# Kernel optimization log

Measured on AMD Instinct MI355X. Metric: run time of the kernel, lower is better.

Reference implementation:

```python
import jax, jax.numpy as jnp
import numpy as np

B, S, D, H = 4, 2048, 512, 8
HD = D // H

def setup_inputs() -> dict:
    key = jax.random.key(0)
    ks = jax.random.split(key, 11)
    sc = 0.02
    inp = {
        'query': jax.random.normal(ks[0], (B, S, D), jnp.float32),
        'key':   jax.random.normal(ks[1], (B, S, D), jnp.float32),
        'value': jax.random.normal(ks[2], (B, S, D), jnp.float32),
        # causal boolean mask, broadcastable to (B, H, S, S)
        'mask':  jnp.tril(jnp.ones((S, S), bool))[None, None],
        'wq': jax.random.normal(ks[3], (D, D), jnp.float32) * sc,
        'bq': jnp.zeros((D,), jnp.float32),
        'wk': jax.random.normal(ks[4], (D, D), jnp.float32) * sc,
        'bk': jnp.zeros((D,), jnp.float32),
        'wv': jax.random.normal(ks[5], (D, D), jnp.float32) * sc,
        'bv': jnp.zeros((D,), jnp.float32),
        'wo': jax.random.normal(ks[6], (D, D), jnp.float32) * sc,
        'bo': jnp.zeros((D,), jnp.float32),
    }
    return inp


def reference(query, key, value, mask, wq, bq, wk, bk, wv, bv, wo, bo):
    b, s, d = query.shape

    def proj(x, w, bias):
        # torch nn.Linear: x @ W^T + b, then split heads -> (B, H, L, HD)
        y = x @ w.T + bias
        return y.reshape(b, -1, H, HD).transpose(0, 2, 1, 3)

    q = proj(query, wq, bq)   # (B,H,S,HD)
    k = proj(key,   wk, bk)
    v = proj(value, wv, bv)

    scores = jnp.einsum('bhqd,bhkd->bhqk', q, k) / np.sqrt(HD).astype(jnp.float32)
    scores = jnp.where(mask, scores, -jnp.inf)
    # torch code subtracts rowmax then softmaxes; jax.nn.softmax is the same stable form
    attn = jax.nn.softmax(scores, axis=-1)  # dropout p=0.0 -> identity
    out = jnp.einsum('bhqk,bhkd->bhqd', attn, v)
    out = out.transpose(0, 2, 1, 3).reshape(b, s, d)
    return out @ wo.T + bo
```

## Files before the change

kernel.cpp:

```cpp
#include <hip/hip_runtime.h>

#define NB 4
#define NS 2048
#define ND 512
#define NH 8
#define NHD 64
#define NM (NB*NS)

using bf16 = __bf16;
using bf16x8 = __bf16 __attribute__((ext_vector_type(8)));
using f32x4 = float __attribute__((ext_vector_type(4)));
using i16x4 = short __attribute__((ext_vector_type(4)));

static_assert(sizeof(bf16x8) == 16, "bf16x8 must be 16B");
static_assert(sizeof(i16x4) == 8, "i16x4 must be 8B");

typedef __attribute__((address_space(1))) void glob_t;
typedef __attribute__((address_space(3))) void lds_t;

__device__ __forceinline__ void mfma16(f32x4& c, i16x4 a, i16x4 b) {
    asm("v_mfma_f32_16x16x16_bf16 %0, %1, %2, %0" : "+v"(c) : "v"(a), "v"(b));
}

__device__ __forceinline__ void stage16_f32(const float* __restrict__ src, bf16* dst) {
    float4 f0 = *(const float4*)(src + 0);
    float4 f1 = *(const float4*)(src + 4);
    float4 f2 = *(const float4*)(src + 8);
    float4 f3 = *(const float4*)(src + 12);
    bf16x8 v0, v1;
    v0[0]=(bf16)f0.x; v0[1]=(bf16)f0.y; v0[2]=(bf16)f0.z; v0[3]=(bf16)f0.w;
    v0[4]=(bf16)f1.x; v0[5]=(bf16)f1.y; v0[6]=(bf16)f1.z; v0[7]=(bf16)f1.w;
    v1[0]=(bf16)f2.x; v1[1]=(bf16)f2.y; v1[2]=(bf16)f2.z; v1[3]=(bf16)f2.w;
    v1[4]=(bf16)f3.x; v1[5]=(bf16)f3.y; v1[6]=(bf16)f3.z; v1[7]=(bf16)f3.w;
    *(bf16x8*)dst       = v0;
    *(bf16x8*)(dst + 8) = v1;
}

template<bool A_BF16, bool HEAD_OUT>
__device__ __forceinline__ void gemm_body(bf16* As, bf16* Bs, const void* __restrict__ Ap,
        const float* __restrict__ W, const float* __restrict__ bias, void* __restrict__ outp)
{
    constexpr int LP = 40;
    const int tid  = threadIdx.x;
    const int lane = tid & 63;
    const int wid  = tid >> 6;
    const int wm = wid >> 1, wn = wid & 1;
    const int lr = lane & 15, lg = lane >> 4;
    const int m0 = blockIdx.x * 128, n0 = blockIdx.y * 128;

    const int srow = tid >> 1;
    const int scol = (tid & 1) << 4;

    f32x4 acc[4][4] = {};

    for (int k0 = 0; k0 < ND; k0 += 32) {
        if (A_BF16) {
            const bf16* src = (const bf16*)Ap + (size_t)(m0 + srow) * ND + k0 + scol;
            *(uint4*)&As[srow * LP + scol]     = *(const uint4*)(src);
            *(uint4*)&As[srow * LP + scol + 8] = *(const uint4*)(src + 8);
        } else {
            const float* src = (const float*)Ap + (size_t)(m0 + srow) * ND + k0 + scol;
            stage16_f32(src, &As[srow * LP + scol]);
        }
        {
            const float* src = W + (size_t)(n0 + srow) * ND + k0 + scol;
            stage16_f32(src, &Bs[srow * LP + scol]);
        }
        __syncthreads();

        bf16x8 af[4], bfr[4];
        #pragma unroll
        for (int i = 0; i < 4; i++)
            af[i] = *(const bf16x8*)&As[(wm * 64 + i * 16 + lr) * LP + lg * 8];
        #pragma unroll
        for (int i = 0; i < 4; i++)
            bfr[i] = *(const bf16x8*)&Bs[(wn * 64 + i * 16 + lr) * LP + lg * 8];

        #pragma unroll
        for (int mf = 0; mf < 4; mf++)
            #pragma unroll
            for (int nf = 0; nf < 4; nf++)
                acc[mf][nf] = __builtin_amdgcn_mfma_f32_16x16x32_bf16(
                        af[mf], bfr[nf], acc[mf][nf], 0, 0, 0);
        __syncthreads();
    }

    float bv[4];
    #pragma unroll
    for (int nf = 0; nf < 4; nf++)
        bv[nf] = bias[n0 + wn * 64 + nf * 16 + lr];

    #pragma unroll
    for (int mf = 0; mf < 4; mf++) {
        #pragma unroll
        for (int nf = 0; nf < 4; nf++) {
            const int col = n0 + wn * 64 + nf * 16 + lr;
            #pragma unroll
            for (int r = 0; r < 4; r++) {
                const int row = m0 + wm * 64 + mf * 16 + lg * 4 + r;
                const float v = acc[mf][nf][r] + bv[nf];
                if (HEAD_OUT) {
                    const int b  = row >> 11;
                    const int s  = row & (NS - 1);
                    const int hh = col >> 6;
                    const int hd = col & (NHD - 1);
                    ((bf16*)outp)[(((size_t)b * NH + hh) * NS + s) * NHD + hd] = (bf16)v;
                } else {
                    ((float*)outp)[(size_t)row * ND + col] = v;
                }
            }
        }
    }
}

__global__ __launch_bounds__(256) void gemm_proj3(
        const float* __restrict__ q, const float* __restrict__ k, const float* __restrict__ v,
        const float* __restrict__ wq, const float* __restrict__ wk, const float* __restrict__ wv,
        const float* __restrict__ bq, const float* __restrict__ bk, const float* __restrict__ bv,
        bf16* __restrict__ qb, bf16* __restrict__ kb, bf16* __restrict__ vb)
{
    __shared__ __align__(16) bf16 As[128 * 40];
    __shared__ __align__(16) bf16 Bs[128 * 40];
    const int z = blockIdx.z;
    const float* A = (z == 0) ? q  : (z == 1) ? k  : v;
    const float* W = (z == 0) ? wq : (z == 1) ? wk : wv;
    const float* B = (z == 0) ? bq : (z == 1) ? bk : bv;
    bf16*        o = (z == 0) ? qb : (z == 1) ? kb : vb;
    gemm_body<false, true>(As, Bs, A, W, B, o);
}

__global__ __launch_bounds__(256) void gemm_out(const bf16* __restrict__ A,
        const float* __restrict__ W, const float* __restrict__ b, float* __restrict__ out)
{
    __shared__ __align__(16) bf16 As[128 * 40];
    __shared__ __align__(16) bf16 Bs[128 * 40];
    gemm_body<true, false>(As, Bs, A, W, b, out);
}

#define QSCALE 0.18033688011112042f

__global__ __launch_bounds__(128) void attn_kern(const bf16* __restrict__ Qg,
        const bf16* __restrict__ Kg, const bf16* __restrict__ Vg,
        bf16* __restrict__ Og)
{
    __shared__ __align__(16) bf16 Kt[2][64 * 64];
    __shared__ __align__(16) bf16 Vt[2][64 * 64];

    const int b = blockIdx.z, h = blockIdx.y;
    const int x = blockIdx.x;
    const int qb = (x & 1) ? ((x - 1) >> 1) : (31 - (x >> 1));
    const int tid = threadIdx.x;
    const int lane = tid & 63, w = tid >> 6;
    const int lr = lane & 15, lg = lane >> 4;

    const size_t bh = ((size_t)b * NH + h) * NS;
    const bf16* Kb = Kg + bh * NHD;
    const bf16* Vb = Vg + bh * NHD;

    int ksrc[4];
    #pragma unroll
    for (int j = 0; j < 4; j++) {
        const int c   = (w * 4 + j) * 64 + lane;
        const int row = c >> 3;
        const int cs  = (c & 7) ^ (row & 7);
        ksrc[j] = row * NHD + cs * 8;
    }

    const int c8 = tid >> 4;
    const int r0 = (tid & 15) * 4;

    bf16x8 qf[2][2];
    #pragma unroll
    for (int rf = 0; rf < 2; rf++) {
        const bf16* qp = Qg + (bh + qb * 64 + w * 32 + rf * 16 + lr) * NHD;
        #pragma unroll
        for (int kk = 0; kk < 2; kk++) {
            bf16x8 t = *(const bf16x8*)(qp + kk * 32 + lg * 8);
            #pragma unroll
            for (int j = 0; j < 8; j++)
                qf[rf][kk][j] = (bf16)((float)t[j] * QSCALE);
        }
    }

    f32x4 acc_o[2][4] = {};
    float l_lane[2] = {0.f, 0.f};

    const int qrow0 = qb * 64 + w * 32;
    const int ntiles = qb + 1;

    auto stage = [&](int buf, int kv0) {
        #pragma unroll
        for (int j = 0; j < 4; j++)
            __builtin_amdgcn_global_load_lds(
                (const glob_t*)(Kb + (size_t)kv0 * NHD + ksrc[j]),
                (lds_t*)(&Kt[buf][(w * 4 + j) * 512]), 16, 0, 0);
        bf16x8 vv[4];
        #pragma unroll
        for (int i = 0; i < 4; i++)
            vv[i] = *(const bf16x8*)(Vb + (size_t)(kv0 + r0 + i) * NHD + c8 * 8);
        #pragma unroll
        for (int j = 0; j < 8; j++) {
            const int hd = c8 * 8 + j;
            int byte = hd * 128 + r0 * 2;
            byte ^= (hd & 7) << 4;
            i16x4 pk;
            #pragma unroll
            for (int i = 0; i < 4; i++) {
                bf16 hval = vv[i][j];
                pk[i] = (short)__builtin_bit_cast(unsigned short, hval);
            }
            *(i16x4*)((char*)&Vt[buf][0] + byte) = pk;
        }
    };

    stage(0, 0);
    __syncthreads();

    int cur = 0;
    for (int t = 0; t < ntiles; t++) {
        const int kv0 = t * 64;
        if (t + 1 < ntiles) stage(cur ^ 1, kv0 + 64);

        f32x4 s[4][2];
        #pragma unroll
        for (int nf = 0; nf < 4; nf++) {
            bf16x8 kf[2];
            #pragma unroll
            for (int kk = 0; kk < 2; kk++) {
                const int row = nf * 16 + lr;
                int byte = row * 128 + (kk * 32 + lg * 8) * 2;
                byte ^= (row & 7) << 4;
                kf[kk] = *(const bf16x8*)((const char*)&Kt[cur][0] + byte);
            }
            #pragma unroll
            for (int rf = 0; rf < 2; rf++) {
                f32x4 a = {};
                a = __builtin_amdgcn_mfma_f32_16x16x32_bf16(kf[0], qf[rf][0], a, 0, 0, 0);
                a = __builtin_amdgcn_mfma_f32_16x16x32_bf16(kf[1], qf[rf][1], a, 0, 0, 0);
                s[nf][rf] = a;
            }
        }

        i16x4 pa[2][4];
        if (kv0 + 63 > qrow0) {
            #pragma unroll
            for (int rf = 0; rf < 2; rf++) {
                const int qg = qrow0 + rf * 16 + lr;
                #pragma unroll
                for (int nf = 0; nf < 4; nf++)
                    #pragma unroll
                    for (int rr = 0; rr < 4; rr++) {
                        const int kvg = kv0 + nf * 16 + lg * 4 + rr;
                        float sv = s[nf][rf][rr];
                        sv = (kvg > qg) ? -1e30f : sv;
                        const float p = __builtin_amdgcn_exp2f(sv);
                        l_lane[rf] += p;
                        bf16 ph = (bf16)p;
                        pa[rf][nf][rr] = (short)__builtin_bit_cast(unsigned short, ph);
                    }
            }
        } else {
            #pragma unroll
            for (int rf = 0; rf < 2; rf++)
                #pragma unroll
                for (int nf = 0; nf < 4; nf++)
                    #pragma unroll
                    for (int rr = 0; rr < 4; rr++) {
                        const float p = __builtin_amdgcn_exp2f(s[nf][rf][rr]);
                        l_lane[rf] += p;
                        bf16 ph = (bf16)p;
                        pa[rf][nf][rr] = (short)__builtin_bit_cast(unsigned short, ph);
                    }
        }

        i16x4 vf[4][4];
        #pragma unroll
        for (int hf = 0; hf < 4; hf++)
            #pragma unroll
            for (int nf = 0; nf < 4; nf++) {
                const int hd = hf * 16 + lr;
                int byte = hd * 128 + (nf * 16 + lg * 4) * 2;
                byte ^= (hd & 7) << 4;
                vf[hf][nf] = *(const i16x4*)((const char*)&Vt[cur][0] + byte);
            }

        __builtin_amdgcn_s_setprio(1);
        #pragma unroll
        for (int rf = 0; rf < 2; rf++)
            #pragma unroll
            for (int hf = 0; hf < 4; hf++)
                #pragma unroll
                for (int nf = 0; nf < 4; nf++)
                    mfma16(acc_o[rf][hf], pa[rf][nf], vf[hf][nf]);
        __builtin_amdgcn_s_setprio(0);

        __syncthreads();
        cur ^= 1;
    }

    #pragma unroll
    for (int rf = 0; rf < 2; rf++) {
        float l = l_lane[rf];
        l += __shfl_xor(l, 16);
        l += __shfl_xor(l, 32);
        const float linv = 1.0f / l;
        #pragma unroll
        for (int rr = 0; rr < 4; rr++) {
            const float li = __shfl(linv, lg * 4 + rr, 16);
            const int row = qrow0 + rf * 16 + lg * 4 + rr;
            #pragma unroll
            for (int hf = 0; hf < 4; hf++) {
                const int col = h * NHD + hf * 16 + lr;
                Og[((size_t)b * NS + row) * ND + col] = (bf16)(acc_o[rf][hf][rr] * li);
            }
        }
    }
}

extern "C" void kernel_launch(void* const* d_in, const int* in_sizes, int n_in,
                              void* d_out, int out_size, void* d_ws, size_t ws_size,
                              hipStream_t stream) {
    const float* query = (const float*)d_in[0];
    const float* key   = (const float*)d_in[1];
    const float* value = (const float*)d_in[2];
    const float* wq = (const float*)d_in[4];
    const float* bq = (const float*)d_in[5];
    const float* wk = (const float*)d_in[6];
    const float* bk = (const float*)d_in[7];
    const float* wv = (const float*)d_in[8];
    const float* bv = (const float*)d_in[9];
    const float* wo = (const float*)d_in[10];
    const float* bo = (const float*)d_in[11];
    float* out = (float*)d_out;

    bf16* qb = (bf16*)d_ws;
    bf16* kb = qb + (size_t)NM * ND;
    bf16* vb = kb + (size_t)NM * ND;
    bf16* ob = vb + (size_t)NM * ND;

    gemm_proj3<<<dim3(NM / 128, ND / 128, 3), 256, 0, stream>>>(
            query, key, value, wq, wk, wv, bq, bk, bv, qb, kb, vb);

    attn_kern<<<dim3(NS / 64, NH, NB), 128, 0, stream>>>(qb, kb, vb, ob);

    gemm_out<<<dim3(NM / 128, ND / 128), 256, 0, stream>>>(ob, wo, bo, out);
}
```

Baseline: 127.1 us.

## Double-buffer GEMM shared-memory tiles with register prefetch of next K tile

The projection and output GEMMs now prefetch the next K-slice of A and W into registers while MFMAs run on the current LDS buffer, then convert and write into the alternate LDS buffer. This cuts one of the two barriers per iteration and hides global load latency behind compute. It doubles LDS use per block and adds register pressure from the prefetched float4 values, which could lower occupancy.

```diff
diff --git a/kernel.cpp b/kernel.cpp
--- a/kernel.cpp
+++ b/kernel.cpp
@@ -22,16 +22,12 @@
     asm("v_mfma_f32_16x16x16_bf16 %0, %1, %2, %0" : "+v"(c) : "v"(a), "v"(b));
 }
 
-__device__ __forceinline__ void stage16_f32(const float* __restrict__ src, bf16* dst) {
-    float4 f0 = *(const float4*)(src + 0);
-    float4 f1 = *(const float4*)(src + 4);
-    float4 f2 = *(const float4*)(src + 8);
-    float4 f3 = *(const float4*)(src + 12);
+__device__ __forceinline__ void cvt16(const float4* f, bf16* dst) {
     bf16x8 v0, v1;
-    v0[0]=(bf16)f0.x; v0[1]=(bf16)f0.y; v0[2]=(bf16)f0.z; v0[3]=(bf16)f0.w;
-    v0[4]=(bf16)f1.x; v0[5]=(bf16)f1.y; v0[6]=(bf16)f1.z; v0[7]=(bf16)f1.w;
-    v1[0]=(bf16)f2.x; v1[1]=(bf16)f2.y; v1[2]=(bf16)f2.z; v1[3]=(bf16)f2.w;
-    v1[4]=(bf16)f3.x; v1[5]=(bf16)f3.y; v1[6]=(bf16)f3.z; v1[7]=(bf16)f3.w;
+    v0[0]=(bf16)f[0].x; v0[1]=(bf16)f[0].y; v0[2]=(bf16)f[0].z; v0[3]=(bf16)f[0].w;
+    v0[4]=(bf16)f[1].x; v0[5]=(bf16)f[1].y; v0[6]=(bf16)f[1].z; v0[7]=(bf16)f[1].w;
+    v1[0]=(bf16)f[2].x; v1[1]=(bf16)f[2].y; v1[2]=(bf16)f[2].z; v1[3]=(bf16)f[2].w;
+    v1[4]=(bf16)f[3].x; v1[5]=(bf16)f[3].y; v1[6]=(bf16)f[3].z; v1[7]=(bf16)f[3].w;
     *(bf16x8*)dst       = v0;
     *(bf16x8*)(dst + 8) = v1;
 }
@@ -40,7 +36,8 @@
 __device__ __forceinline__ void gemm_body(bf16* As, bf16* Bs, const void* __restrict__ Ap,
         const float* __restrict__ W, const float* __restrict__ bias, void* __restrict__ outp)
 {
-    constexpr int LP = 40;
+    constexpr int LP  = 40;
+    constexpr int BUF = 128 * LP;
     const int tid  = threadIdx.x;
     const int lane = tid & 63;
     const int wid  = tid >> 6;
@@ -53,28 +50,55 @@
 
     f32x4 acc[4][4] = {};
 
-    for (int k0 = 0; k0 < ND; k0 += 32) {
+    float4 fa[4], fb[4];
+    uint4  ua[2];
+
+    auto load_tile = [&](int k0) {
         if (A_BF16) {
             const bf16* src = (const bf16*)Ap + (size_t)(m0 + srow) * ND + k0 + scol;
-            *(uint4*)&As[srow * LP + scol]     = *(const uint4*)(src);
-            *(uint4*)&As[srow * LP + scol + 8] = *(const uint4*)(src + 8);
+            ua[0] = *(const uint4*)(src);
+            ua[1] = *(const uint4*)(src + 8);
         } else {
             const float* src = (const float*)Ap + (size_t)(m0 + srow) * ND + k0 + scol;
-            stage16_f32(src, &As[srow * LP + scol]);
-        }
-        {
-            const float* src = W + (size_t)(n0 + srow) * ND + k0 + scol;
-            stage16_f32(src, &Bs[srow * LP + scol]);
-        }
-        __syncthreads();
+            fa[0] = *(const float4*)(src + 0);
+            fa[1] = *(const float4*)(src + 4);
+            fa[2] = *(const float4*)(src + 8);
+            fa[3] = *(const float4*)(src + 12);
+        }
+        const float* wsrc = W + (size_t)(n0 + srow) * ND + k0 + scol;
+        fb[0] = *(const float4*)(wsrc + 0);
+        fb[1] = *(const float4*)(wsrc + 4);
+        fb[2] = *(const float4*)(wsrc + 8);
+        fb[3] = *(const float4*)(wsrc + 12);
+    };
+    auto write_tile = [&](int buf) {
+        bf16* da = As + buf * BUF + srow * LP + scol;
+        if (A_BF16) {
+            *(uint4*)da       = ua[0];
+            *(uint4*)(da + 8) = ua[1];
+        } else {
+            cvt16(fa, da);
+        }
+        cvt16(fb, Bs + buf * BUF + srow * LP + scol);
+    };
+
+    load_tile(0);
+    write_tile(0);
+    __syncthreads();
+
+    int cur = 0;
+    #pragma unroll 2
+    for (int t = 0; t < ND / 32; t++) {
+        const int k0 = t * 32;
+        if (t < ND / 32 - 1) load_tile(k0 + 32);
 
         bf16x8 af[4], bfr[4];
         #pragma unroll
         for (int i = 0; i < 4; i++)
-            af[i] = *(const bf16x8*)&As[(wm * 64 + i * 16 + lr) * LP + lg * 8];
+            af[i] = *(const bf16x8*)&As[cur * BUF + (wm * 64 + i * 16 + lr) * LP + lg * 8];
         #pragma unroll
         for (int i = 0; i < 4; i++)
-            bfr[i] = *(const bf16x8*)&Bs[(wn * 64 + i * 16 + lr) * LP + lg * 8];
+            bfr[i] = *(const bf16x8*)&Bs[cur * BUF + (wn * 64 + i * 16 + lr) * LP + lg * 8];
 
         #pragma unroll
         for (int mf = 0; mf < 4; mf++)
@@ -82,7 +106,10 @@
             for (int nf = 0; nf < 4; nf++)
                 acc[mf][nf] = __builtin_amdgcn_mfma_f32_16x16x32_bf16(
                         af[mf], bfr[nf], acc[mf][nf], 0, 0, 0);
+
+        if (t < ND / 32 - 1) write_tile(cur ^ 1);
         __syncthreads();
+        cur ^= 1;
     }
 
     float bv[4];
@@ -119,8 +146,8 @@
         const float* __restrict__ bq, const float* __restrict__ bk, const float* __restrict__ bv,
         bf16* __restrict__ qb, bf16* __restrict__ kb, bf16* __restrict__ vb)
 {
-    __shared__ __align__(16) bf16 As[128 * 40];
-    __shared__ __align__(16) bf16 Bs[128 * 40];
+    __shared__ __align__(16) bf16 As[2 * 128 * 40];
+    __shared__ __align__(16) bf16 Bs[2 * 128 * 40];
     const int z = blockIdx.z;
     const float* A = (z == 0) ? q  : (z == 1) ? k  : v;
     const float* W = (z == 0) ? wq : (z == 1) ? wk : wv;
@@ -132,8 +159,8 @@
 __global__ __launch_bounds__(256) void gemm_out(const bf16* __restrict__ A,
         const float* __restrict__ W, const float* __restrict__ b, float* __restrict__ out)
 {
-    __shared__ __align__(16) bf16 As[128 * 40];
-    __shared__ __align__(16) bf16 Bs[128 * 40];
+    __shared__ __align__(16) bf16 As[2 * 128 * 40];
+    __shared__ __align__(16) bf16 Bs[2 * 128 * 40];
     gemm_body<true, false>(As, Bs, A, W, b, out);
 }
 
```

New measurement: 128.9 us. Within noise of the previous version (+1.4%).
